# Optimization experiments

Hardware: AMD Instinct MI355X
Metric: run time of the kernel (lower is better)

Reference implementation:

```python
import jax, jax.numpy as jnp
import numpy as np

SIN, TEMB, EMB, S = 128, 512, 1024, 64
BATCH, T = 4, 4096


def setup_inputs() -> dict:
    key = jax.random.key(0)
    ks = jax.random.split(key, 16)

    def w(k, *shape):
        return jax.random.normal(k, shape, jnp.float32) / np.float32(np.sqrt(shape[0]))

    return {
        "time_embed": jax.random.normal(ks[0], (SIN,), jnp.float32),
        "x": jax.random.normal(ks[1], (BATCH, T, EMB), jnp.float32),
        "W1": w(ks[2], SIN, TEMB), "b1": jnp.zeros((TEMB,), jnp.float32),
        "W2": w(ks[3], TEMB, TEMB), "b2": jnp.zeros((TEMB,), jnp.float32),
        "WA": w(ks[4], TEMB, S), "bA": jnp.zeros((S,), jnp.float32),
        "WB": w(ks[5], TEMB, S, EMB), "bB": jnp.zeros((S, EMB), jnp.float32),
        "WC": w(ks[6], TEMB, EMB, S), "bC": jnp.zeros((EMB, S), jnp.float32),
        "WD": w(ks[7], TEMB, EMB), "bD": jnp.zeros((EMB,), jnp.float32),
        "Wdl": w(ks[8], TEMB, S), "bdl": jnp.zeros((S,), jnp.float32),
        "MA": w(ks[9], SIN, S), "mA": jnp.zeros((S,), jnp.float32),
        "MB": w(ks[10], SIN, S, EMB), "mB": jnp.zeros((S, EMB), jnp.float32),
        "MC": w(ks[11], SIN, EMB, S), "mC": jnp.zeros((EMB, S), jnp.float32),
        "MD": w(ks[12], SIN, EMB), "mD": jnp.zeros((EMB,), jnp.float32),
        "Mdl": w(ks[13], SIN, S), "mdl": jnp.zeros((S,), jnp.float32),
    }


def _ssm_forward(time_embed, x, W1, b1, W2, b2, WA, bA, WB, bB, WC, bC, WD, bD,
                 Wdl, bdl, MA, mA, MB, mB, MC, mC, MD, mD, Mdl, mdl):
    # time-dependent parameter generation
    t = jax.nn.silu(time_embed @ W1 + b1)
    t = t @ W2 + b2  # [TEMB]

    A_base = -jax.nn.softplus(t @ WA + bA)                       # [S]
    B_base = jnp.einsum('t,tse->se', t, WB) + bB                 # [S,E]
    C_base = jnp.einsum('t,tes->es', t, WC) + bC                 # [E,S]
    D_base = t @ WD + bD                                         # [E]
    delta_base = jax.nn.softplus(t @ Wdl + bdl) + 1e-4           # [S]

    A = A_base * jax.nn.sigmoid(time_embed @ MA + mA)
    Bm = B_base * jax.nn.sigmoid(jnp.einsum('t,tse->se', time_embed, MB) + mB)
    C = C_base * jax.nn.sigmoid(jnp.einsum('t,tes->es', time_embed, MC) + mC)
    D = D_base * jax.nn.sigmoid(time_embed @ MD + mD)
    delta = delta_base * jax.nn.sigmoid(time_embed @ Mdl + mdl)  # [S]

    A_bar = jnp.exp(delta * A)          # [S]
    B_bar = delta[:, None] * Bm         # [S,E]

    xt = jnp.swapaxes(x, 0, 1)          # [T,B,E]

    def step(h, x_t):                   # h: [B,S], x_t: [B,E]
        h_new = A_bar * h + x_t @ B_bar.T
        y = h_new @ C.T                 # [B,E]
        return h_new, y

    h0 = jnp.zeros((x.shape[0], A_bar.shape[0]), x.dtype)
    _, ys = jax.lax.scan(step, h0, xt)  # ys: [T,B,E]
    return jnp.swapaxes(ys, 0, 1) + D * x


def reference(time_embed, x, W1, b1, W2, b2, WA, bA, WB, bB, WC, bC, WD, bD,
              Wdl, bdl, MA, mA, MB, mB, MC, mC, MD, mD, Mdl, mdl):
    return _ssm_forward(time_embed, x, W1, b1, W2, b2, WA, bA, WB, bB, WC, bC,
                        WD, bD, Wdl, bdl, MA, mA, MB, mB, MC, mC, MD, mD, Mdl, mdl)
```

## Files before the change

kernel.cpp:

```cpp
#include <hip/hip_runtime.h>
#include <math.h>

#define SIN_ 128
#define TEMB_ 512
#define EMB_ 1024
#define S_ 64
#define B_ 4
#define T_ 4096
#define NROW (B_*T_)
#define L_ 64
#define NC_ (T_/L_)

#define GK 32
#define NSL 32
#define SLW 512
#define NCH 16
#define NGCH 4

#define WS_T1     0
#define WS_T2     512
#define WS_DELTA  1024
#define WS_ABAR   1088
#define WS_EL     1152
#define WS_FAC    1216
#define WS_D      5312
#define WS_BMTH   6336
#define WS_CTH    39104
#define WS_PD     71872
#define WS_PDG    88256
#define WS_PA     92352
#define WS_PDL    92480
#define WS_PBF    92608
#define WS_HLOCH  92608
#define WS_CHEND  1403328
#define WS_CARRY  1419712

typedef float nt4 __attribute__((ext_vector_type(4)));

__device__ __forceinline__ float sigmoidf_(float x){ return 1.f/(1.f+expf(-x)); }
__device__ __forceinline__ float softplusf_(float x){ return x>20.f ? x : log1pf(expf(x)); }
__device__ __forceinline__ float4 sig4_(float4 g){
  float4 r; r.x=sigmoidf_(g.x); r.y=sigmoidf_(g.y); r.z=sigmoidf_(g.z); r.w=sigmoidf_(g.w); return r;
}
__device__ __forceinline__ unsigned short f2bf(float x){
  unsigned int u = __float_as_uint(x);
  unsigned int r = (u + 0x7FFFu + ((u>>16)&1u)) >> 16;
  return (unsigned short)r;
}
__device__ __forceinline__ ushort4 pack4nt(nt4 v){
  return make_ushort4(f2bf(v.x),f2bf(v.y),f2bf(v.z),f2bf(v.w));
}
__device__ __forceinline__ float bf2f(unsigned short h){
  return __uint_as_float(((unsigned int)h)<<16);
}
__device__ __forceinline__ nt4 ntload(const float4* p){
  return __builtin_nontemporal_load((const nt4*)p);
}
__device__ __forceinline__ void ntstore(float* p, float4 v){
  nt4 t = {v.x, v.y, v.z, v.w};
  __builtin_nontemporal_store(t, (nt4*)p);
}

__global__ void k_t1(const float* __restrict__ te, const float* __restrict__ W1,
                     const float* __restrict__ b1, float* __restrict__ ws){
  __shared__ float ste[SIN_];
  int tid = threadIdx.x;
  ste[tid] = te[tid]; ste[tid+64] = te[tid+64];
  __syncthreads();
  int j = blockIdx.x*64 + tid;
  float a = b1[j];
  #pragma unroll 16
  for (int i=0;i<SIN_;i++) a += ste[i]*W1[i*TEMB_ + j];
  ws[WS_T1 + j] = a * sigmoidf_(a);
}

__global__ __launch_bounds__(512) void k_t2(const float* __restrict__ W2,
                                            const float* __restrict__ b2,
                                            float* __restrict__ ws){
  __shared__ float st1[TEMB_];
  __shared__ float red[8][64];
  int tid = threadIdx.x;
  st1[tid] = ws[WS_T1 + tid];
  __syncthreads();
  int jl = tid & 63, kc = tid >> 6;
  int j = blockIdx.x*64 + jl;
  float p = 0.f;
  #pragma unroll 8
  for (int i=0;i<64;i++){
    int k = kc*64 + i;
    p += st1[k]*W2[k*TEMB_ + j];
  }
  red[kc][jl] = p;
  __syncthreads();
  if (tid < 64){
    float a = b2[blockIdx.x*64 + tid];
    #pragma unroll
    for (int c=0;c<8;c++) a += red[c][tid];
    ws[WS_T2 + blockIdx.x*64 + tid] = a;
  }
}

__global__ __launch_bounds__(256,2) void k_partial(
    const float* __restrict__ te,
    const float* __restrict__ WB, const float* __restrict__ MB,
    const float* __restrict__ WC, const float* __restrict__ MC,
    const float* __restrict__ WD, const float* __restrict__ MD,
    const float* __restrict__ WA, const float* __restrict__ MA,
    const float* __restrict__ Wdl, const float* __restrict__ Mdl,
    float* __restrict__ ws){
  __shared__ float st2[TEMB_];
  __shared__ float ste[SIN_];
  int tid = threadIdx.x;
  st2[tid] = ws[WS_T2 + tid];
  st2[tid+256] = ws[WS_T2 + tid + 256];
  if (tid < SIN_) ste[tid] = te[tid];
  __syncthreads();
  unsigned short* pbf = (unsigned short*)(ws + WS_PBF);
  int bb = blockIdx.x;
  if (bb < 1024){
    int r = bb>>9, rem = bb&511, j = rem>>4, c = rem&15;
    const float4* W4 = (const float4*)(r ? WC : WB);
    const float4* base = W4 + (size_t)(c*GK)*16384 + j*SLW + tid;
    const float* coef = st2 + c*GK;
    nt4 a0={0,0,0,0}, a1={0,0,0,0};
    #pragma unroll 8
    for (int k=0;k<GK;k++){
      const float4* p = base + (size_t)k*16384;
      nt4 w0=ntload(p), w1=ntload(p+256);
      float cv = coef[k];
      a0 += cv*w0; a1 += cv*w1;
    }
    ushort4* dst = (ushort4*)pbf + (size_t)((r*NSL+j)*NCH + c)*SLW;
    dst[tid]     = pack4nt(a0);
    dst[tid+256] = pack4nt(a1);
  } else if (bb < 1280){
    int g = bb-1024, r = g>>7, rem = g&127, j = rem>>2, cg = rem&3;
    const float4* M4 = (const float4*)(r ? MC : MB);
    const float4* base = M4 + (size_t)(cg*GK)*16384 + j*SLW + tid;
    const float* coef = ste + cg*GK;
    nt4 a0={0,0,0,0}, a1={0,0,0,0};
    #pragma unroll 8
    for (int k=0;k<GK;k++){
      const float4* p = base + (size_t)k*16384;
      nt4 w0=ntload(p), w1=ntload(p+256);
      float cv = coef[k];
      a0 += cv*w0; a1 += cv*w1;
    }
    ushort4* dst = (ushort4*)pbf + (size_t)524288 + (size_t)((r*NSL+j)*NGCH + cg)*SLW;
    dst[tid]     = pack4nt(a0);
    dst[tid+256] = pack4nt(a1);
  } else if (bb < 1296){
    int c = bb-1280;
    const float4* base = (const float4*)WD + (size_t)(c*GK)*256 + tid;
    const float* coef = st2 + c*GK;
    nt4 a={0,0,0,0};
    #pragma unroll 4
    for (int k=0;k<GK;k++){
      nt4 w = ntload(base + (size_t)k*256);
      a += coef[k]*w;
    }
    float4 af = make_float4(a.x,a.y,a.z,a.w);
    ((float4*)(ws + WS_PD))[c*256 + tid] = af;
  } else if (bb < 1300){
    int cg = bb-1296;
    const float4* base = (const float4*)MD + (size_t)(cg*GK)*256 + tid;
    const float* coef = ste + cg*GK;
    nt4 a={0,0,0,0};
    #pragma unroll 4
    for (int k=0;k<GK;k++){
      nt4 w = ntload(base + (size_t)k*256);
      a += coef[k]*w;
    }
    float4 af = make_float4(a.x,a.y,a.z,a.w);
    ((float4*)(ws + WS_PDG))[cg*256 + tid] = af;
  } else {
    const float* Wm = (bb==1300) ? WA : Wdl;
    const float* Mm = (bb==1300) ? MA : Mdl;
    int outbase = (bb==1300) ? WS_PA : WS_PDL;
    __shared__ float red[16][68];
    int q = tid&15, kr = tid>>4;
    float4 acc={0,0,0,0};
    const float4* W4 = (const float4*)Wm;
    #pragma unroll 4
    for (int it=0; it<32; ++it){
      int k = it*16 + kr;
      float4 w = W4[k*16 + q];
      float cv = st2[k];
      acc.x=fmaf(cv,w.x,acc.x); acc.y=fmaf(cv,w.y,acc.y); acc.z=fmaf(cv,w.z,acc.z); acc.w=fmaf(cv,w.w,acc.w);
    }
    red[kr][4*q+0]=acc.x; red[kr][4*q+1]=acc.y; red[kr][4*q+2]=acc.z; red[kr][4*q+3]=acc.w;
    __syncthreads();
    if (tid < 64){
      float s = 0.f;
      #pragma unroll
      for (int g=0;g<16;g++) s += red[g][tid];
      ws[outbase + tid] = s;
    }
    __syncthreads();
    float4 gac={0,0,0,0};
    const float4* M4 = (const float4*)Mm;
    #pragma unroll 4
    for (int it=0; it<8; ++it){
      int k = it*16 + kr;
      float4 w = M4[k*16 + q];
      float cv = ste[k];
      gac.x=fmaf(cv,w.x,gac.x); gac.y=fmaf(cv,w.y,gac.y); gac.z=fmaf(cv,w.z,gac.z); gac.w=fmaf(cv,w.w,gac.w);
    }
    red[kr][4*q+0]=gac.x; red[kr][4*q+1]=gac.y; red[kr][4*q+2]=gac.z; red[kr][4*q+3]=gac.w;
    __syncthreads();
    if (tid < 64){
      float s = 0.f;
      #pragma unroll
      for (int g=0;g<16;g++) s += red[g][tid];
      ws[outbase + 64 + tid] = s;
    }
  }
}

__global__ __launch_bounds__(256) void k_finalize(
    const float* __restrict__ bB, const float* __restrict__ mB,
    const float* __restrict__ bC, const float* __restrict__ mC,
    const float* __restrict__ bD, const float* __restrict__ mD,
    const float* __restrict__ bA_, const float* __restrict__ mA_,
    const float* __restrict__ bdl, const float* __restrict__ mdl,
    float* __restrict__ ws){
  int tid = threadIdx.x, bb = blockIdx.x;
  const ushort4* pbf4 = (const ushort4*)(ws + WS_PBF);
  unsigned short* bmth = (unsigned short*)(ws + WS_BMTH);
  unsigned short* cth  = (unsigned short*)(ws + WS_CTH);
  if (bb < 128){
    int r = bb>>6;
    int q = (bb&63)*256 + tid;
    int j = q>>9, p = q&511;
    float4 a = {0,0,0,0};
    size_t wbase = ((size_t)(r*NSL+j)*NCH)*SLW + p;
    #pragma unroll
    for (int c=0;c<NCH;c++){
      ushort4 v = pbf4[wbase + (size_t)c*SLW];
      a.x += bf2f(v.x); a.y += bf2f(v.y); a.z += bf2f(v.z); a.w += bf2f(v.w);
    }
    float4 g = {0,0,0,0};
    size_t gbase = (size_t)524288 + ((size_t)(r*NSL+j)*NGCH)*SLW + p;
    #pragma unroll
    for (int cg=0;cg<NGCH;cg++){
      ushort4 v = pbf4[gbase + (size_t)cg*SLW];
      g.x += bf2f(v.x); g.y += bf2f(v.y); g.z += bf2f(v.z); g.w += bf2f(v.w);
    }
    if (r == 0){
      float4 b4 = ((const float4*)bB)[q];
      float4 m4 = ((const float4*)mB)[q];
      float4 sg = sig4_(make_float4(g.x+m4.x, g.y+m4.y, g.z+m4.z, g.w+m4.w));
      float4 v = make_float4((a.x+b4.x)*sg.x,(a.y+b4.y)*sg.y,(a.z+b4.z)*sg.z,(a.w+b4.w)*sg.w);
      int o = q*4; int s = o>>10; int e = o&1023;
      bmth[(e+0)*64 + s] = f2bf(v.x);
      bmth[(e+1)*64 + s] = f2bf(v.y);
      bmth[(e+2)*64 + s] = f2bf(v.z);
      bmth[(e+3)*64 + s] = f2bf(v.w);
    } else {
      float4 b4 = ((const float4*)bC)[q];
      float4 m4 = ((const float4*)mC)[q];
      float4 sg = sig4_(make_float4(g.x+m4.x, g.y+m4.y, g.z+m4.z, g.w+m4.w));
      float4 v = make_float4((a.x+b4.x)*sg.x,(a.y+b4.y)*sg.y,(a.z+b4.z)*sg.z,(a.w+b4.w)*sg.w);
      int o = q*4; int e = o>>6; int s = o&63;
      cth[(s+0)*1024 + e] = f2bf(v.x);
      cth[(s+1)*1024 + e] = f2bf(v.y);
      cth[(s+2)*1024 + e] = f2bf(v.z);
      cth[(s+3)*1024 + e] = f2bf(v.w);
    }
  } else if (bb == 128){
    float4 a = {0,0,0,0};
    #pragma unroll
    for (int c=0;c<NCH;c++){
      float4 v = ((const float4*)(ws + WS_PD))[c*256 + tid];
      a.x+=v.x; a.y+=v.y; a.z+=v.z; a.w+=v.w;
    }
    float4 g = {0,0,0,0};
    #pragma unroll
    for (int cg=0;cg<NGCH;cg++){
      float4 v = ((const float4*)(ws + WS_PDG))[cg*256 + tid];
      g.x+=v.x; g.y+=v.y; g.z+=v.z; g.w+=v.w;
    }
    float4 b4 = ((const float4*)bD)[tid];
    float4 m4 = ((const float4*)mD)[tid];
    float4 sg = sig4_(make_float4(g.x+m4.x, g.y+m4.y, g.z+m4.z, g.w+m4.w));
    float4 v = make_float4((a.x+b4.x)*sg.x,(a.y+b4.y)*sg.y,(a.z+b4.z)*sg.z,(a.w+b4.w)*sg.w);
    ((float4*)(ws + WS_D))[tid] = v;
  } else {
    __shared__ float sda[64];
    if (tid < 64){
      int s = tid;
      float A = -softplusf_(ws[WS_PA+s] + bA_[s]) * sigmoidf_(ws[WS_PA+64+s] + mA_[s]);
      float delta = (softplusf_(ws[WS_PDL+s] + bdl[s]) + 1e-4f) * sigmoidf_(ws[WS_PDL+64+s] + mdl[s]);
      float da = delta * A;
      sda[s] = da;
      ws[WS_DELTA+s] = delta;
      ws[WS_ABAR+s]  = expf(da);
      ws[WS_EL+s]    = expf((float)L_*da);
    }
    __syncthreads();
    for (int idx=tid; idx<L_*S_; idx+=256){
      int tl = idx>>6, s = idx&63;
      ws[WS_FAC+idx] = expf((float)(tl+1)*sda[s]);
    }
  }
}

__global__ __launch_bounds__(256) void k_scan(const float* __restrict__ x, float* __restrict__ ws){
  __shared__ float Xs[64][68];
  __shared__ float BsT[64][68];
  __shared__ float Us[64][65];
  __shared__ float sdl[S_], sab[S_];
  int tid = threadIdx.x;
  int bb = blockIdx.x;
  int row0 = (bb>>6)*T_ + (bb&63)*L_;
  if (tid<64){ sdl[tid]=ws[WS_DELTA+tid]; sab[tid]=ws[WS_ABAR+tid]; }
  float acc[4][4];
  #pragma unroll
  for (int i=0;i<4;i++)
    #pragma unroll
    for (int j=0;j<4;j++) acc[i][j]=0.f;
  int ty = tid>>4, tx = tid&15;
  const float4* x4 = (const float4*)x;
  const ushort4* bm4 = (const ushort4*)(ws + WS_BMTH);
  for (int kk=0; kk<EMB_; kk+=64){
    #pragma unroll
    for (int t=0;t<4;t++){
      int fl = t*256+tid; int rr = fl>>4, cq = fl&15;
      float4 xv = x4[(size_t)(row0+rr)*256 + (kk>>2) + cq];
      *(float4*)&Xs[rr][cq*4] = xv;
      ushort4 hv = bm4[(size_t)(kk+rr)*16 + cq];
      *(float4*)&BsT[rr][cq*4] = make_float4(bf2f(hv.x),bf2f(hv.y),bf2f(hv.z),bf2f(hv.w));
    }
    __syncthreads();
    #pragma unroll 8
    for (int k=0;k<64;k++){
      float4 b4 = *(const float4*)&BsT[k][4*tx];
      float x0 = Xs[4*ty+0][k], x1 = Xs[4*ty+1][k], x2 = Xs[4*ty+2][k], x3 = Xs[4*ty+3][k];
      acc[0][0]+=x0*b4.x; acc[0][1]+=x0*b4.y; acc[0][2]+=x0*b4.z; acc[0][3]+=x0*b4.w;
      acc[1][0]+=x1*b4.x; acc[1][1]+=x1*b4.y; acc[1][2]+=x1*b4.z; acc[1][3]+=x1*b4.w;
      acc[2][0]+=x2*b4.x; acc[2][1]+=x2*b4.y; acc[2][2]+=x2*b4.z; acc[2][3]+=x2*b4.w;
      acc[3][0]+=x3*b4.x; acc[3][1]+=x3*b4.y; acc[3][2]+=x3*b4.z; acc[3][3]+=x3*b4.w;
    }
    __syncthreads();
  }
  #pragma unroll
  for (int i=0;i<4;i++)
    #pragma unroll
    for (int j=0;j<4;j++)
      Us[4*ty+i][4*tx+j] = acc[i][j]*sdl[4*tx+j];
  __syncthreads();
  if (tid<64){
    unsigned short* hh = (unsigned short*)(ws + WS_HLOCH);
    int s = tid; float h = 0.f, ab = sab[s];
    #pragma unroll 8
    for (int t=0;t<L_;t++){
      h = fmaf(ab, h, Us[t][s]);
      hh[(size_t)(row0+t)*S_ + s] = f2bf(h);
    }
    ws[WS_CHEND + bb*S_ + s] = h;
  }
}

__global__ __launch_bounds__(256) void k_carry(float* __restrict__ ws){
  __shared__ float ch[B_*NC_*S_];
  int tid = threadIdx.x;
  const float4* src = (const float4*)(ws + WS_CHEND);
  float4* chv = (float4*)ch;
  for (int i=tid;i<4096;i+=256) chv[i] = src[i];
  __syncthreads();
  int b = tid>>6, s = tid&63;
  float el = ws[WS_EL + s];
  float carry = 0.f;
  #pragma unroll 8
  for (int c=0;c<NC_;c++){
    int idx = (b*NC_ + c)*S_ + s;
    float v = ch[idx];
    ch[idx] = carry;
    carry = fmaf(el, carry, v);
  }
  __syncthreads();
  float4* dst = (float4*)(ws + WS_CARRY);
  for (int i=tid;i<4096;i+=256) dst[i] = chv[i];
}

__global__ __launch_bounds__(256) void k_out(const float* __restrict__ x,
                                             const float* __restrict__ ws,
                                             float* __restrict__ out){
  __shared__ float Cts[64][68];
  __shared__ float Hs[128][68];
  int tid = threadIdx.x;
  int bb = blockIdx.x;
  int rt = bb & 127, et = bb >> 7;
  int row0 = rt*128, e0 = et*64;
  int b = row0 >> 12;
  int cbase = b*NC_ + ((row0 & (T_-1)) >> 6);
  const ushort4* hl4h = (const ushort4*)(ws + WS_HLOCH);
  const ushort4* cth4 = (const ushort4*)(ws + WS_CTH);
  const float4* fc4 = (const float4*)(ws + WS_FAC);
  const float4* cr4 = (const float4*)(ws + WS_CARRY);
  #pragma unroll
  for (int t=0;t<8;t++){
    int fl = t*256+tid; int rr = fl>>4, q = fl&15;
    ushort4 h4 = hl4h[(size_t)(row0+rr)*16 + q];
    float4 f = fc4[(rr & (L_-1))*16 + q];
    float4 c = cr4[(cbase + (rr>>6))*16 + q];
    float4 hv = make_float4(bf2f(h4.x)+f.x*c.x, bf2f(h4.y)+f.y*c.y,
                            bf2f(h4.z)+f.z*c.z, bf2f(h4.w)+f.w*c.w);
    *(float4*)&Hs[rr][q*4] = hv;
  }
  #pragma unroll
  for (int t=0;t<4;t++){
    int fl = t*256+tid; int rr = fl>>4, q = fl&15;
    ushort4 ct4 = cth4[(size_t)rr*256 + (e0>>2) + q];
    *(float4*)&Cts[rr][q*4] = make_float4(bf2f(ct4.x),bf2f(ct4.y),bf2f(ct4.z),bf2f(ct4.w));
  }
  __syncthreads();
  int ty = tid>>4, tx = tid&15;
  float acc[8][4];
  #pragma unroll
  for (int i=0;i<8;i++)
    #pragma unroll
    for (int j=0;j<4;j++) acc[i][j]=0.f;
  #pragma unroll 4
  for (int s=0;s<64;s++){
    float4 c4 = *(const float4*)&Cts[s][4*tx];
    #pragma unroll
    for (int i=0;i<8;i++){
      float hv = Hs[8*ty+i][s];
      acc[i][0]+=hv*c4.x; acc[i][1]+=hv*c4.y; acc[i][2]+=hv*c4.z; acc[i][3]+=hv*c4.w;
    }
  }
  float4 d4 = ((const float4*)(ws + WS_D))[(e0>>2) + tx];
  #pragma unroll
  for (int i=0;i<8;i++){
    int row = row0 + 8*ty + i;
    float4 x4v = reinterpret_cast<const float4*>(x + (size_t)row*EMB_ + e0)[tx];
    float4 o;
    o.x = acc[i][0] + d4.x*x4v.x;
    o.y = acc[i][1] + d4.y*x4v.y;
    o.z = acc[i][2] + d4.z*x4v.z;
    o.w = acc[i][3] + d4.w*x4v.w;
    ntstore(out + (size_t)row*EMB_ + e0 + 4*tx, o);
  }
}

extern "C" void kernel_launch(void* const* d_in, const int* in_sizes, int n_in,
                              void* d_out, int out_size, void* d_ws, size_t ws_size,
                              hipStream_t stream){
  const float* te  = (const float*)d_in[0];
  const float* x   = (const float*)d_in[1];
  const float* W1  = (const float*)d_in[2];
  const float* b1  = (const float*)d_in[3];
  const float* W2  = (const float*)d_in[4];
  const float* b2  = (const float*)d_in[5];
  const float* WA  = (const float*)d_in[6];
  const float* bA  = (const float*)d_in[7];
  const float* WB  = (const float*)d_in[8];
  const float* bB  = (const float*)d_in[9];
  const float* WC  = (const float*)d_in[10];
  const float* bC  = (const float*)d_in[11];
  const float* WD  = (const float*)d_in[12];
  const float* bD  = (const float*)d_in[13];
  const float* Wdl = (const float*)d_in[14];
  const float* bdl = (const float*)d_in[15];
  const float* MA  = (const float*)d_in[16];
  const float* mA  = (const float*)d_in[17];
  const float* MB  = (const float*)d_in[18];
  const float* mB  = (const float*)d_in[19];
  const float* MC  = (const float*)d_in[20];
  const float* mC  = (const float*)d_in[21];
  const float* MD  = (const float*)d_in[22];
  const float* mD  = (const float*)d_in[23];
  const float* Mdl = (const float*)d_in[24];
  const float* mdl = (const float*)d_in[25];
  float* ws  = (float*)d_ws;
  float* out = (float*)d_out;

  k_t1<<<8,64,0,stream>>>(te, W1, b1, ws);
  k_t2<<<8,512,0,stream>>>(W2, b2, ws);
  k_partial<<<1302,256,0,stream>>>(te, WB,MB, WC,MC, WD,MD, WA,MA, Wdl,Mdl, ws);
  k_finalize<<<130,256,0,stream>>>(bB,mB, bC,mC, bD,mD, bA,mA, bdl,mdl, ws);
  k_scan<<<256,256,0,stream>>>(x, ws);
  k_carry<<<1,256,0,stream>>>(ws);
  k_out<<<2048,256,0,stream>>>(x, ws, out);
}
```

Before: 159.6 us.

## Fuse chunk-carry scan into output kernel and shrink row tile to 64

Removes the single-block k_carry kernel and its workspace round trip. Each k_out block now serially recomputes its own inter-chunk carry from the chunk-end states with 64 threads. Row tiles shrink from 128 to 64 so that each block covers exactly one chunk, which doubles the grid to 4096 blocks and halves per-thread accumulators. This saves a launch and a serial dependency, but adds redundant per-block carry loops of up to 63 dependent steps, reloads the C tile twice as often, and adds an extra barrier.

```diff
diff --git a/kernel.cpp b/kernel.cpp
--- a/kernel.cpp
+++ b/kernel.cpp
@@ -33,7 +33,6 @@
 #define WS_PBF    92608
 #define WS_HLOCH  92608
 #define WS_CHEND  1403328
-#define WS_CARRY  1419712
 
 typedef float nt4 __attribute__((ext_vector_type(4)));
 
@@ -361,52 +360,28 @@
   }
 }
 
-__global__ __launch_bounds__(256) void k_carry(float* __restrict__ ws){
-  __shared__ float ch[B_*NC_*S_];
-  int tid = threadIdx.x;
-  const float4* src = (const float4*)(ws + WS_CHEND);
-  float4* chv = (float4*)ch;
-  for (int i=tid;i<4096;i+=256) chv[i] = src[i];
-  __syncthreads();
-  int b = tid>>6, s = tid&63;
-  float el = ws[WS_EL + s];
-  float carry = 0.f;
-  #pragma unroll 8
-  for (int c=0;c<NC_;c++){
-    int idx = (b*NC_ + c)*S_ + s;
-    float v = ch[idx];
-    ch[idx] = carry;
-    carry = fmaf(el, carry, v);
-  }
-  __syncthreads();
-  float4* dst = (float4*)(ws + WS_CARRY);
-  for (int i=tid;i<4096;i+=256) dst[i] = chv[i];
-}
-
 __global__ __launch_bounds__(256) void k_out(const float* __restrict__ x,
                                              const float* __restrict__ ws,
                                              float* __restrict__ out){
   __shared__ float Cts[64][68];
-  __shared__ float Hs[128][68];
+  __shared__ float Hs[64][68];
+  __shared__ float sc[64];
   int tid = threadIdx.x;
   int bb = blockIdx.x;
-  int rt = bb & 127, et = bb >> 7;
-  int row0 = rt*128, e0 = et*64;
+  int rt = bb & 255, et = bb >> 8;
+  int row0 = rt*64, e0 = et*64;
   int b = row0 >> 12;
-  int cbase = b*NC_ + ((row0 & (T_-1)) >> 6);
+  int c = (row0 & (T_-1)) >> 6;
   const ushort4* hl4h = (const ushort4*)(ws + WS_HLOCH);
   const ushort4* cth4 = (const ushort4*)(ws + WS_CTH);
   const float4* fc4 = (const float4*)(ws + WS_FAC);
-  const float4* cr4 = (const float4*)(ws + WS_CARRY);
-  #pragma unroll
-  for (int t=0;t<8;t++){
-    int fl = t*256+tid; int rr = fl>>4, q = fl&15;
-    ushort4 h4 = hl4h[(size_t)(row0+rr)*16 + q];
-    float4 f = fc4[(rr & (L_-1))*16 + q];
-    float4 c = cr4[(cbase + (rr>>6))*16 + q];
-    float4 hv = make_float4(bf2f(h4.x)+f.x*c.x, bf2f(h4.y)+f.y*c.y,
-                            bf2f(h4.z)+f.z*c.z, bf2f(h4.w)+f.w*c.w);
-    *(float4*)&Hs[rr][q*4] = hv;
+  if (tid < 64){
+    float el = ws[WS_EL + tid];
+    float carry = 0.f;
+    const float* ch = ws + WS_CHEND + (size_t)b*NC_*S_ + tid;
+    for (int cp=0; cp<c; ++cp)
+      carry = fmaf(el, carry, ch[(size_t)cp*S_]);
+    sc[tid] = carry;
   }
   #pragma unroll
   for (int t=0;t<4;t++){
@@ -415,25 +390,36 @@
     *(float4*)&Cts[rr][q*4] = make_float4(bf2f(ct4.x),bf2f(ct4.y),bf2f(ct4.z),bf2f(ct4.w));
   }
   __syncthreads();
+  #pragma unroll
+  for (int t=0;t<4;t++){
+    int fl = t*256+tid; int rr = fl>>4, q = fl&15;
+    ushort4 h4 = hl4h[(size_t)(row0+rr)*16 + q];
+    float4 f = fc4[rr*16 + q];
+    float4 cv = *(const float4*)&sc[4*q];
+    float4 hv = make_float4(bf2f(h4.x)+f.x*cv.x, bf2f(h4.y)+f.y*cv.y,
+                            bf2f(h4.z)+f.z*cv.z, bf2f(h4.w)+f.w*cv.w);
+    *(float4*)&Hs[rr][q*4] = hv;
+  }
+  __syncthreads();
   int ty = tid>>4, tx = tid&15;
-  float acc[8][4];
-  #pragma unroll
-  for (int i=0;i<8;i++)
+  float acc[4][4];
+  #pragma unroll
+  for (int i=0;i<4;i++)
     #pragma unroll
     for (int j=0;j<4;j++) acc[i][j]=0.f;
-  #pragma unroll 4
+  #pragma unroll 8
   for (int s=0;s<64;s++){
     float4 c4 = *(const float4*)&Cts[s][4*tx];
-    #pragma unroll
-    for (int i=0;i<8;i++){
-      float hv = Hs[8*ty+i][s];
-      acc[i][0]+=hv*c4.x; acc[i][1]+=hv*c4.y; acc[i][2]+=hv*c4.z; acc[i][3]+=hv*c4.w;
-    }
+    float h0 = Hs[4*ty+0][s], h1 = Hs[4*ty+1][s], h2 = Hs[4*ty+2][s], h3 = Hs[4*ty+3][s];
+    acc[0][0]+=h0*c4.x; acc[0][1]+=h0*c4.y; acc[0][2]+=h0*c4.z; acc[0][3]+=h0*c4.w;
+    acc[1][0]+=h1*c4.x; acc[1][1]+=h1*c4.y; acc[1][2]+=h1*c4.z; acc[1][3]+=h1*c4.w;
+    acc[2][0]+=h2*c4.x; acc[2][1]+=h2*c4.y; acc[2][2]+=h2*c4.z; acc[2][3]+=h2*c4.w;
+    acc[3][0]+=h3*c4.x; acc[3][1]+=h3*c4.y; acc[3][2]+=h3*c4.z; acc[3][3]+=h3*c4.w;
   }
   float4 d4 = ((const float4*)(ws + WS_D))[(e0>>2) + tx];
   #pragma unroll
-  for (int i=0;i<8;i++){
-    int row = row0 + 8*ty + i;
+  for (int i=0;i<4;i++){
+    int row = row0 + 4*ty + i;
     float4 x4v = reinterpret_cast<const float4*>(x + (size_t)row*EMB_ + e0)[tx];
     float4 o;
     o.x = acc[i][0] + d4.x*x4v.x;
@@ -481,6 +467,5 @@
   k_partial<<<1302,256,0,stream>>>(te, WB,MB, WC,MC, WD,MD, WA,MA, Wdl,Mdl, ws);
   k_finalize<<<130,256,0,stream>>>(bB,mB, bC,mC, bD,mD, bA,mA, bdl,mdl, ws);
   k_scan<<<256,256,0,stream>>>(x, ws);
-  k_carry<<<1,256,0,stream>>>(ws);
-  k_out<<<2048,256,0,stream>>>(x, ws, out);
-}
+  k_out<<<4096,256,0,stream>>>(x, ws, out);
+}
```

Result: slower. 176.1 us (+10.3%).
